# Optimization experiments

Hardware: AMD Instinct MI355X
Metric: run time of the kernel (lower is better)

## Reference

```python
import jax, jax.numpy as jnp
import numpy as np

B, C, T, H, W = 4, 256, 8, 32, 32
EPS = 1e-6


def setup_inputs() -> dict:
    key = jax.random.key(0)
    ks = jax.random.split(key, 8)
    s = 0.02  # init scale for 1x1 conv weights
    return {
        "x_motion": jax.random.normal(ks[0], (B, C, T, H, W), jnp.float32),
        "x_ref": jax.random.normal(ks[1], (B, C, 1, H, W), jnp.float32),
        "gamma": jnp.ones((C,), jnp.float32),
        "beta": jnp.zeros((C,), jnp.float32),
        "Wq": jax.random.normal(ks[2], (C, C), jnp.float32) * s,
        "bq": jnp.zeros((C,), jnp.float32),
        "Wk": jax.random.normal(ks[3], (C, C), jnp.float32) * s,
        "bk": jnp.zeros((C,), jnp.float32),
        "Wv": jax.random.normal(ks[4], (C, C), jnp.float32) * s,
        "bv": jnp.zeros((C,), jnp.float32),
        "Wo": jax.random.normal(ks[5], (C, C), jnp.float32) * s,
        "bo": jnp.zeros((C,), jnp.float32),
    }


def _group_norm(x, gamma, beta):
    # GroupNorm(num_groups=1): normalize over (C,T,H,W) per sample
    mu = jnp.mean(x, axis=(1, 2, 3, 4), keepdims=True)
    var = jnp.var(x, axis=(1, 2, 3, 4), keepdims=True)
    xn = (x - mu) * jax.lax.rsqrt(var + EPS)
    return xn * gamma[None, :, None, None, None] + beta[None, :, None, None, None]


def _conv1(x, Wmat, bias):
    # 1x1x1 Conv3d == per-position channel matmul
    return jnp.einsum('oc,bcthw->bothw', Wmat, x) + bias[None, :, None, None, None]


def reference(x_motion, x_ref, gamma, beta, Wq, bq, Wk, bk, Wv, bv, Wo, bo):
    h_mot = _group_norm(x_motion, gamma, beta)
    h_ref = _group_norm(x_ref, gamma, beta)
    q = _conv1(h_mot, Wq, bq)   # [b,c,t,h,w]
    k = _conv1(h_ref, Wk, bk)   # [b,c,1,h,w]
    v = _conv1(h_ref, Wv, bv)
    b, c, t, h, w = q.shape
    qf = q.transpose(0, 2, 3, 4, 1).reshape(b, t, h * w, c)   # [b,t,hw,c]
    kf = k[:, :, 0].transpose(0, 2, 3, 1).reshape(b, h * w, c)  # [b,hw,c]
    vf = v[:, :, 0].transpose(0, 2, 3, 1).reshape(b, h * w, c)
    # cross-attention: every frame attends to the single reference frame
    attn = jnp.einsum('btqc,bkc->btqk', qf, kf) * (c ** -0.5)
    attn = jax.nn.softmax(attn, axis=-1)
    out = jnp.einsum('btqk,bkc->btqc', attn, vf)
    out = out.reshape(b, t, h, w, c).transpose(0, 4, 1, 2, 3)  # [b,c,t,h,w]
    return x_motion + _conv1(out, Wo, bo)
```

## Files before the change

kernel.cpp:

```cpp
#include <hip/hip_runtime.h>
#include <math.h>
#include <stdint.h>

#define B_   4
#define C_   256
#define T_   8
#define HW_  1024
#define PM_  8192
#define PR_  1024
#define NM_  (C_ * PM_)
#define NR_  (C_ * PR_)
#define NBM  128
#define NBR  16
#define EPS_ 1e-6f

typedef unsigned short u16;
typedef unsigned int u32;
typedef __attribute__((ext_vector_type(8))) short short8;
typedef __attribute__((ext_vector_type(4))) float f32x4;

__device__ inline u16 f2bf(float f) {
    uint32_t u = __builtin_bit_cast(uint32_t, f);
    u += 0x7fffu + ((u >> 16) & 1u);
    return (u16)(u >> 16);
}
__device__ inline u32 pk2bf(float a, float b) {
    return (u32)f2bf(a) | ((u32)f2bf(b) << 16);
}

__device__ inline f32x4 mfma16(short8 a, short8 b, f32x4 c) {
    f32x4 d;
    asm("v_mfma_f32_16x16x32_bf16 %0, %1, %2, %3" : "=v"(d) : "v"(a), "v"(b), "0"(c));
    return d;
}
__device__ __forceinline__ short8 lds8(const char* p) {
    return __builtin_bit_cast(short8, *(const uint4*)p);
}
__device__ __forceinline__ void gl16(const void* g, void* l) {
    __builtin_amdgcn_global_load_lds(
        reinterpret_cast<const uint32_t __attribute__((address_space(1)))*>(
            reinterpret_cast<uintptr_t>(g)),
        reinterpret_cast<uint32_t __attribute__((address_space(3)))*>(
            reinterpret_cast<uintptr_t>(l)),
        16, 0, 0);
}

__global__ __launch_bounds__(256) void gn_stats(const float* __restrict__ x,
                                                int per_sample, int nblk,
                                                float* __restrict__ part) {
    int b   = blockIdx.x / nblk;
    int blk = blockIdx.x % nblk;
    const float* xb = x + (size_t)b * per_sample;
    int chunk = per_sample / nblk;
    int base  = blk * chunk;
    float s = 0.f, s2 = 0.f;
    for (int i = threadIdx.x * 4; i < chunk; i += 256 * 4) {
        float4 v = *(const float4*)(xb + base + i);
        s  += v.x + v.y + v.z + v.w;
        s2 += v.x * v.x + v.y * v.y + v.z * v.z + v.w * v.w;
    }
    #pragma unroll
    for (int off = 32; off; off >>= 1) {
        s  += __shfl_down(s, off);
        s2 += __shfl_down(s2, off);
    }
    __shared__ float red[8];
    int wid = threadIdx.x >> 6, lane = threadIdx.x & 63;
    if (lane == 0) { red[wid * 2] = s; red[wid * 2 + 1] = s2; }
    __syncthreads();
    if (threadIdx.x == 0) {
        for (int w = 1; w < 4; ++w) { s += red[w * 2]; s2 += red[w * 2 + 1]; }
        part[(size_t)(b * nblk + blk) * 2]     = s;
        part[(size_t)(b * nblk + blk) * 2 + 1] = s2;
    }
}

__global__ __launch_bounds__(256) void gn_finalize(const float* __restrict__ part_m,
                                                   const float* __restrict__ part_r,
                                                   const float* __restrict__ gamma,
                                                   const float* __restrict__ beta,
                                                   float* __restrict__ am, float* __restrict__ dm,
                                                   float* __restrict__ ar, float* __restrict__ dr) {
    int c = threadIdx.x;
    float g = gamma[c], be = beta[c];
    for (int b = 0; b < B_; ++b) {
        float s = 0.f, s2 = 0.f;
        for (int i = 0; i < NBM; ++i) { s += part_m[(b * NBM + i) * 2]; s2 += part_m[(b * NBM + i) * 2 + 1]; }
        float mu   = s / (float)NM_;
        float var  = s2 / (float)NM_ - mu * mu;
        float rstd = rsqrtf(var + EPS_);
        am[b * C_ + c] = rstd * g;
        dm[b * C_ + c] = be - mu * rstd * g;

        s = 0.f; s2 = 0.f;
        for (int i = 0; i < NBR; ++i) { s += part_r[(b * NBR + i) * 2]; s2 += part_r[(b * NBR + i) * 2 + 1]; }
        mu   = s / (float)NR_;
        var  = s2 / (float)NR_ - mu * mu;
        rstd = rsqrtf(var + EPS_);
        ar[b * C_ + c] = rstd * g;
        dr[b * C_ + c] = be - mu * rstd * g;
    }
}

__global__ __launch_bounds__(256) void w2bf(const float* __restrict__ W0,
                                            const float* __restrict__ W1,
                                            const float* __restrict__ W2,
                                            const float* __restrict__ W3,
                                            u16* __restrict__ dst) {
    int idx = blockIdx.x * 256 + threadIdx.x;
    int m = idx >> 13, off = (idx & 8191) * 8;
    const float* s = (m == 0 ? W0 : m == 1 ? W1 : m == 2 ? W2 : W3) + off;
    float4 a = *(const float4*)s, b = *(const float4*)(s + 4);
    ushort4 lo; lo.x = f2bf(a.x); lo.y = f2bf(a.y); lo.z = f2bf(a.z); lo.w = f2bf(a.w);
    ushort4 hi; hi.x = f2bf(b.x); hi.y = f2bf(b.y); hi.z = f2bf(b.z); hi.w = f2bf(b.w);
    *(ushort4*)(dst + m * 65536 + off)     = lo;
    *(ushort4*)(dst + m * 65536 + off + 4) = hi;
}

template<int P>
__global__ __launch_bounds__(256) void norm_tr(const float* __restrict__ X,
                                               const float* __restrict__ alpha,
                                               const float* __restrict__ delta,
                                               u16* __restrict__ Y) {
    __shared__ __align__(16) u16 S[64 * 256];
    int b = blockIdx.z, p0 = blockIdx.x * 64;
    int tid = threadIdx.x;
    #pragma unroll
    for (int pass = 0; pass < 4; ++pass) {
        int qi = pass * 256 + tid;
        int cq = qi & 63, pq = qi >> 6;
        float4 v[4];
        #pragma unroll
        for (int j = 0; j < 4; ++j) {
            int c = cq * 4 + j;
            v[j] = *(const float4*)(X + ((size_t)b * C_ + c) * P + p0 + pq * 4);
            float a = alpha[b * C_ + c], d = delta[b * C_ + c];
            v[j].x = v[j].x * a + d; v[j].y = v[j].y * a + d;
            v[j].z = v[j].z * a + d; v[j].w = v[j].w * a + d;
        }
        #pragma unroll
        for (int jj = 0; jj < 4; ++jj) {
            ushort4 o;
            o.x = f2bf(((const float*)&v[0])[jj]);
            o.y = f2bf(((const float*)&v[1])[jj]);
            o.z = f2bf(((const float*)&v[2])[jj]);
            o.w = f2bf(((const float*)&v[3])[jj]);
            *(ushort4*)&S[(pq * 4 + jj) * 256 + cq * 4] = o;
        }
    }
    __syncthreads();
    const char* Sb = (const char*)S;
    #pragma unroll
    for (int pass = 0; pass < 8; ++pass) {
        int i = pass * 256 + tid;
        int p = i >> 5, s = i & 31;
        uint4 d = *(const uint4*)(Sb + p * 512 + s * 16);
        *(uint4*)((char*)(Y + ((size_t)b * P + p0 + p) * C_) + s * 16) = d;
    }
}

template<int OUT>
__global__ __launch_bounds__(256) void convA(const u16* __restrict__ Xb,
                                             const u16* __restrict__ Wb,
                                             const float* __restrict__ bias,
                                             const float* __restrict__ resid,
                                             void* __restrict__ Yv,
                                             int P, float oscale) {
    __shared__ __align__(16) char lds[65536];
    int b = blockIdx.z, p0 = blockIdx.x * 64, o0 = blockIdx.y * 64;
    int tid = threadIdx.x, w = tid >> 6, l = tid & 63, lg = l >> 4, ln = l & 15;
    int wm = w >> 1, wn = w & 1;
    const char* Xg = (const char*)(Xb + ((size_t)b * P + p0) * C_);
    const char* Wg = (const char*)(Wb + (size_t)o0 * C_);
    #pragma unroll
    for (int i = 0; i < 8; ++i) {
        int ci = i * 4 + w;
        int d = ci * 1024 + l * 16;
        int srco = (d & ~511) | ((d & 511) ^ (((d >> 9) & 7) << 4));
        gl16(Xg + srco, lds + ci * 1024);
        gl16(Wg + srco, lds + 32768 + ci * 1024);
    }
    asm volatile("s_waitcnt vmcnt(0)" ::: "memory");
    __syncthreads();

    f32x4 acc[2][2];
    #pragma unroll
    for (int mm = 0; mm < 2; ++mm)
        #pragma unroll
        for (int nn = 0; nn < 2; ++nn) acc[mm][nn] = (f32x4)0.f;

    #pragma unroll
    for (int f = 0; f < 8; ++f) {
        short8 xf[2], wf[2];
        #pragma unroll
        for (int nn = 0; nn < 2; ++nn) {
            int p = wn * 32 + nn * 16 + ln;
            xf[nn] = lds8(lds + p * 512 + ((f * 64 + lg * 16) ^ ((p & 7) << 4)));
        }
        #pragma unroll
        for (int mm = 0; mm < 2; ++mm) {
            int o = wm * 32 + mm * 16 + ln;
            wf[mm] = lds8(lds + 32768 + o * 512 + ((f * 64 + lg * 16) ^ ((o & 7) << 4)));
        }
        #pragma unroll
        for (int mm = 0; mm < 2; ++mm)
            #pragma unroll
            for (int nn = 0; nn < 2; ++nn) {
                if (OUT == 1) acc[mm][nn] = mfma16(xf[nn], wf[mm], acc[mm][nn]);
                else          acc[mm][nn] = mfma16(wf[mm], xf[nn], acc[mm][nn]);
            }
    }
    __syncthreads();

    if constexpr (OUT == 0) {
        #pragma unroll
        for (int mm = 0; mm < 2; ++mm) {
            int obase = o0 + wm * 32 + mm * 16 + lg * 4;
            float b0 = bias[obase], b1 = bias[obase + 1], b2 = bias[obase + 2], b3 = bias[obase + 3];
            #pragma unroll
            for (int nn = 0; nn < 2; ++nn) {
                int pl = wn * 32 + nn * 16 + ln;
                int a = pl * 128 + ((wm * 64 + mm * 32 + lg * 8) ^ ((pl & 7) << 4));
                *(u32*)(lds + a)     = pk2bf((acc[mm][nn][0] + b0) * oscale, (acc[mm][nn][1] + b1) * oscale);
                *(u32*)(lds + a + 4) = pk2bf((acc[mm][nn][2] + b2) * oscale, (acc[mm][nn][3] + b3) * oscale);
            }
        }
        __syncthreads();
        u16* Y = (u16*)Yv;
        #pragma unroll
        for (int pass = 0; pass < 2; ++pass) {
            int i = pass * 256 + tid;
            int pl = i >> 3, s = i & 7;
            uint4 d = *(const uint4*)(lds + pl * 128 + ((s * 16) ^ ((pl & 7) << 4)));
            *(uint4*)(Y + (size_t)(b * P + p0 + pl) * C_ + o0 + s * 8) = d;
        }
    } else if constexpr (OUT == 1) {
        #pragma unroll
        for (int mm = 0; mm < 2; ++mm) {
            int ol = wm * 32 + mm * 16 + ln;
            float bo = bias[o0 + ol];
            #pragma unroll
            for (int nn = 0; nn < 2; ++nn) {
                int a = ol * 128 + ((wn * 64 + nn * 32 + lg * 8) ^ ((ol & 7) << 4));
                *(u32*)(lds + a)     = pk2bf(acc[mm][nn][0] + bo, acc[mm][nn][1] + bo);
                *(u32*)(lds + a + 4) = pk2bf(acc[mm][nn][2] + bo, acc[mm][nn][3] + bo);
            }
        }
        __syncthreads();
        u16* Y = (u16*)Yv;
        #pragma unroll
        for (int pass = 0; pass < 2; ++pass) {
            int i = pass * 256 + tid;
            int ol = i >> 3, s = i & 7;
            uint4 d = *(const uint4*)(lds + ol * 128 + ((s * 16) ^ ((ol & 7) << 4)));
            *(uint4*)(Y + (size_t)(b * C_ + o0 + ol) * P + p0 + s * 8) = d;
        }
    } else {
        #pragma unroll
        for (int mm = 0; mm < 2; ++mm) {
            int obase = wm * 32 + mm * 16 + lg * 4;
            #pragma unroll
            for (int r = 0; r < 4; ++r) {
                int ol = obase + r;
                float bo = bias[o0 + ol];
                #pragma unroll
                for (int nn = 0; nn < 2; ++nn) {
                    int a = ol * 256 + ((wn * 128 + nn * 64 + ln * 4) ^ ((ol & 7) << 4));
                    *(float*)(lds + a) = acc[mm][nn][r] + bo;
                }
            }
        }
        __syncthreads();
        float* Y = (float*)Yv;
        #pragma unroll
        for (int pass = 0; pass < 4; ++pass) {
            int i = pass * 256 + tid;
            int ol = i >> 4, s = i & 15;
            f32x4 dv = *(const f32x4*)(lds + ol * 256 + ((s * 16) ^ ((ol & 7) << 4)));
            size_t go = (size_t)(b * C_ + o0 + ol) * P + p0 + s * 4;
            float4 rv = *(const float4*)(resid + go);
            float4 o4;
            o4.x = dv[0] + rv.x; o4.y = dv[1] + rv.y; o4.z = dv[2] + rv.z; o4.w = dv[3] + rv.w;
            *(float4*)(Y + go) = o4;
        }
    }
}

__global__ __launch_bounds__(256) void attn2(const u16* __restrict__ qT,
                                             const u16* __restrict__ kT,
                                             const u16* __restrict__ vh,
                                             u16* __restrict__ ao) {
    __shared__ __align__(16) char lds[69632];
    int b = blockIdx.z, t = blockIdx.y, q0 = blockIdx.x * 64;
    int tid = threadIdx.x, w = tid >> 6, l = tid & 63, lg = l >> 4, ln = l & 15;

    const u16* Qrow = qT + ((size_t)b * PM_ + t * HW_ + q0 + w * 16 + ln) * C_;
    short8 qf[8];
    #pragma unroll
    for (int f = 0; f < 8; ++f)
        qf[f] = __builtin_bit_cast(short8, *(const uint4*)((const char*)Qrow + f * 64 + lg * 16));

    const char* Kb = (const char*)(kT + (size_t)b * PR_ * C_);
    const char* Vb = (const char*)(vh + (size_t)b * C_ * PR_);

    f32x4 acc[16];
    #pragma unroll
    for (int cc = 0; cc < 16; ++cc) acc[cc] = (f32x4)0.f;
    float m_r = -1e30f, l_r = 0.f;

    auto stage = [&](int buf, int kt) {
        const char* Kg = Kb + kt * 32 * 512;
        char* Kl = lds + buf * 16384;
        char* Vl = lds + 32768 + buf * 16384;
        #pragma unroll
        for (int i = 0; i < 4; ++i) {
            int ci = i * 4 + w;
            int d = ci * 1024 + l * 16;
            int srco = (d & ~511) | ((d & 511) ^ (((d >> 9) & 7) << 4));
            gl16(Kg + srco, Kl + ci * 1024);
        }
        #pragma unroll
        for (int i = 0; i < 4; ++i) {
            int ci = i * 4 + w;
            int d = ci * 1024 + l * 16;
            int c = d >> 6;
            int srco = c * 2048 + kt * 64 + ((d & 63) ^ (((c >> 1) & 3) << 4));
            gl16(Vb + srco, Vl + ci * 1024);
        }
    };

    stage(0, 0);
    asm volatile("s_waitcnt vmcnt(0)" ::: "memory");
    __syncthreads();

    char* Pl = lds + 65536 + w * 1024;
    for (int kt = 0; kt < 32; ++kt) {
        int buf = kt & 1;
        if (kt < 31) stage(buf ^ 1, kt + 1);
        const char* Kl = lds + buf * 16384;
        const char* Vl = lds + 32768 + buf * 16384;

        f32x4 s0 = (f32x4)0.f, s1 = (f32x4)0.f;
        #pragma unroll
        for (int f = 0; f < 8; ++f) {
            int r1 = 16 + ln;
            short8 k0f = lds8(Kl + ln * 512 + ((f * 64 + lg * 16) ^ ((ln & 7) << 4)));
            short8 k1f = lds8(Kl + r1 * 512 + ((f * 64 + lg * 16) ^ ((r1 & 7) << 4)));
            s0 = mfma16(k0f, qf[f], s0);
            s1 = mfma16(k1f, qf[f], s1);
        }

        float tm = fmaxf(fmaxf(fmaxf(s0[0], s0[1]), fmaxf(s0[2], s0[3])),
                         fmaxf(fmaxf(s1[0], s1[1]), fmaxf(s1[2], s1[3])));
        tm = fmaxf(tm, __shfl_xor(tm, 16));
        tm = fmaxf(tm, __shfl_xor(tm, 32));
        if (__any(tm > m_r + 8.f)) {
            float mn = fmaxf(m_r, tm);
            float sc = __expf(m_r - mn);
            m_r = mn; l_r *= sc;
            #pragma unroll
            for (int cc = 0; cc < 16; ++cc) {
                acc[cc][0] *= sc; acc[cc][1] *= sc; acc[cc][2] *= sc; acc[cc][3] *= sc;
            }
        }
        float p0v[4], p1v[4], rs = 0.f;
        #pragma unroll
        for (int r = 0; r < 4; ++r) { p0v[r] = __expf(s0[r] - m_r); rs += p0v[r]; }
        #pragma unroll
        for (int r = 0; r < 4; ++r) { p1v[r] = __expf(s1[r] - m_r); rs += p1v[r]; }
        rs += __shfl_xor(rs, 16);
        rs += __shfl_xor(rs, 32);
        l_r += rs;

        int sw = ((ln >> 1) & 3) << 4;
        int a0 = ln * 64 + ((lg * 8) ^ sw);
        *(u32*)(Pl + a0)     = pk2bf(p0v[0], p0v[1]);
        *(u32*)(Pl + a0 + 4) = pk2bf(p0v[2], p0v[3]);
        int a1 = ln * 64 + ((32 + lg * 8) ^ sw);
        *(u32*)(Pl + a1)     = pk2bf(p1v[0], p1v[1]);
        *(u32*)(Pl + a1 + 4) = pk2bf(p1v[2], p1v[3]);

        short8 pf = lds8(Pl + ln * 64 + ((lg * 16) ^ sw));

        #pragma unroll
        for (int cc = 0; cc < 16; ++cc) {
            int c = cc * 16 + ln;
            short8 vf = lds8(Vl + c * 64 + ((lg * 16) ^ (((c >> 1) & 3) << 4)));
            acc[cc] = mfma16(vf, pf, acc[cc]);
        }

        asm volatile("s_waitcnt vmcnt(0)" ::: "memory");
        __syncthreads();
    }

    float invl = 1.f / l_r;
    char* Os = lds;
    int qrow = w * 16 + ln;
    #pragma unroll
    for (int cc = 0; cc < 16; ++cc) {
        int a = qrow * 512 + ((cc * 32 + lg * 8) ^ ((qrow & 7) << 4));
        *(u32*)(Os + a)     = pk2bf(acc[cc][0] * invl, acc[cc][1] * invl);
        *(u32*)(Os + a + 4) = pk2bf(acc[cc][2] * invl, acc[cc][3] * invl);
    }
    __syncthreads();
    u16* aob = ao + ((size_t)b * PM_ + t * HW_ + q0) * C_;
    #pragma unroll
    for (int pass = 0; pass < 8; ++pass) {
        int i = pass * 256 + tid;
        int qr = i >> 5, s = i & 31;
        uint4 d = *(const uint4*)(Os + qr * 512 + ((s * 16) ^ ((qr & 7) << 4)));
        *(uint4*)((char*)(aob + (size_t)qr * C_) + s * 16) = d;
    }
}

extern "C" void kernel_launch(void* const* d_in, const int* in_sizes, int n_in,
                              void* d_out, int out_size, void* d_ws, size_t ws_size,
                              hipStream_t stream) {
    const float* x_motion = (const float*)d_in[0];
    const float* x_ref    = (const float*)d_in[1];
    const float* gamma    = (const float*)d_in[2];
    const float* beta     = (const float*)d_in[3];
    const float* Wq = (const float*)d_in[4];
    const float* bq = (const float*)d_in[5];
    const float* Wk = (const float*)d_in[6];
    const float* bk = (const float*)d_in[7];
    const float* Wv = (const float*)d_in[8];
    const float* bv = (const float*)d_in[9];
    const float* Wo = (const float*)d_in[10];
    const float* bo = (const float*)d_in[11];
    float* out = (float*)d_out;
    char* base = (char*)d_ws;

    float* part_m = (float*)(base);
    float* part_r = (float*)(base + 4096);
    float* am = (float*)(base + 8192);
    float* dm = (float*)(base + 12288);
    float* ar = (float*)(base + 16384);
    float* dr = (float*)(base + 20480);
    u16* wall = (u16*)(base + 32768);
    u16* wqb = wall;
    u16* wkb = wall + 65536;
    u16* wvb = wall + 131072;
    u16* wob = wall + 196608;
    u16* xnm = (u16*)(base + 1048576);
    u16* aoh = xnm;
    u16* xnr = (u16*)(base + 1048576 + 16777216);
    u16* qT  = (u16*)(base + 1048576 + 16777216 + 2097152);
    u16* kTp = (u16*)(base + 1048576 + 2 * 16777216 + 2097152);
    u16* vh  = (u16*)(base + 1048576 + 2 * 16777216 + 2 * 2097152);

    gn_stats<<<dim3(B_ * NBM), 256, 0, stream>>>(x_motion, NM_, NBM, part_m);
    gn_stats<<<dim3(B_ * NBR), 256, 0, stream>>>(x_ref, NR_, NBR, part_r);
    gn_finalize<<<dim3(1), 256, 0, stream>>>(part_m, part_r, gamma, beta, am, dm, ar, dr);
    w2bf<<<dim3(128), 256, 0, stream>>>(Wq, Wk, Wv, Wo, wall);

    norm_tr<PM_><<<dim3(PM_ / 64, 1, B_), 256, 0, stream>>>(x_motion, am, dm, xnm);
    norm_tr<PR_><<<dim3(PR_ / 64, 1, B_), 256, 0, stream>>>(x_ref, ar, dr, xnr);

    convA<0><<<dim3(PM_ / 64, 4, B_), 256, 0, stream>>>(xnm, wqb, bq, nullptr, qT, PM_, 0.0625f);
    convA<0><<<dim3(PR_ / 64, 4, B_), 256, 0, stream>>>(xnr, wkb, bk, nullptr, kTp, PR_, 1.f);
    convA<1><<<dim3(PR_ / 64, 4, B_), 256, 0, stream>>>(xnr, wvb, bv, nullptr, vh, PR_, 1.f);

    attn2<<<dim3(16, T_, B_), 256, 0, stream>>>(qT, kTp, vh, aoh);

    convA<2><<<dim3(PM_ / 64, 4, B_), 256, 0, stream>>>(aoh, wob, bo, x_motion, out, PM_, 1.f);
}
```

Baseline: 144.1 us.

## Merge small launches and rewrite attention with 32x32 MFMA and larger tiles

```diff
diff --git a/kernel.cpp b/kernel.cpp
--- a/kernel.cpp
+++ b/kernel.cpp
@@ -13,11 +13,13 @@
 #define NBM  128
 #define NBR  16
 #define EPS_ 1e-6f
+#define QSCALE 0.09016844f
 
 typedef unsigned short u16;
 typedef unsigned int u32;
 typedef __attribute__((ext_vector_type(8))) short short8;
 typedef __attribute__((ext_vector_type(4))) float f32x4;
+typedef __attribute__((ext_vector_type(16))) float f32x16;
 
 __device__ inline u16 f2bf(float f) {
     uint32_t u = __builtin_bit_cast(uint32_t, f);
@@ -31,6 +33,11 @@
 __device__ inline f32x4 mfma16(short8 a, short8 b, f32x4 c) {
     f32x4 d;
     asm("v_mfma_f32_16x16x32_bf16 %0, %1, %2, %3" : "=v"(d) : "v"(a), "v"(b), "0"(c));
+    return d;
+}
+__device__ inline f32x16 mfma32(short8 a, short8 b, f32x16 c) {
+    f32x16 d;
+    asm("v_mfma_f32_32x32x16_bf16 %0, %1, %2, %3" : "=v"(d) : "v"(a), "v"(b), "0"(c));
     return d;
 }
 __device__ __forceinline__ short8 lds8(const char* p) {
@@ -45,11 +52,10 @@
         16, 0, 0);
 }
 
-__global__ __launch_bounds__(256) void gn_stats(const float* __restrict__ x,
-                                                int per_sample, int nblk,
-                                                float* __restrict__ part) {
-    int b   = blockIdx.x / nblk;
-    int blk = blockIdx.x % nblk;
+__device__ void gn_body(const float* __restrict__ x, int per_sample, int nblk,
+                        float* __restrict__ part, int bid) {
+    int b   = bid / nblk;
+    int blk = bid % nblk;
     const float* xb = x + (size_t)b * per_sample;
     int chunk = per_sample / nblk;
     int base  = blk * chunk;
@@ -74,39 +80,47 @@
         part[(size_t)(b * nblk + blk) * 2 + 1] = s2;
     }
 }
-
-__global__ __launch_bounds__(256) void gn_finalize(const float* __restrict__ part_m,
-                                                   const float* __restrict__ part_r,
-                                                   const float* __restrict__ gamma,
-                                                   const float* __restrict__ beta,
-                                                   float* __restrict__ am, float* __restrict__ dm,
-                                                   float* __restrict__ ar, float* __restrict__ dr) {
-    int c = threadIdx.x;
-    float g = gamma[c], be = beta[c];
-    for (int b = 0; b < B_; ++b) {
-        float s = 0.f, s2 = 0.f;
-        for (int i = 0; i < NBM; ++i) { s += part_m[(b * NBM + i) * 2]; s2 += part_m[(b * NBM + i) * 2 + 1]; }
-        float mu   = s / (float)NM_;
-        float var  = s2 / (float)NM_ - mu * mu;
-        float rstd = rsqrtf(var + EPS_);
-        am[b * C_ + c] = rstd * g;
-        dm[b * C_ + c] = be - mu * rstd * g;
-
-        s = 0.f; s2 = 0.f;
-        for (int i = 0; i < NBR; ++i) { s += part_r[(b * NBR + i) * 2]; s2 += part_r[(b * NBR + i) * 2 + 1]; }
-        mu   = s / (float)NR_;
-        var  = s2 / (float)NR_ - mu * mu;
-        rstd = rsqrtf(var + EPS_);
-        ar[b * C_ + c] = rstd * g;
-        dr[b * C_ + c] = be - mu * rstd * g;
-    }
-}
-
-__global__ __launch_bounds__(256) void w2bf(const float* __restrict__ W0,
-                                            const float* __restrict__ W1,
-                                            const float* __restrict__ W2,
-                                            const float* __restrict__ W3,
-                                            u16* __restrict__ dst) {
+__global__ __launch_bounds__(256) void gn_all(const float* __restrict__ xm,
+                                              const float* __restrict__ xr,
+                                              float* __restrict__ part_m,
+                                              float* __restrict__ part_r) {
+    if (blockIdx.x < 512) gn_body(xm, NM_, NBM, part_m, blockIdx.x);
+    else                  gn_body(xr, NR_, NBR, part_r, blockIdx.x - 512);
+}
+
+__global__ __launch_bounds__(256) void fin_w2bf(const float* __restrict__ part_m,
+                                                const float* __restrict__ part_r,
+                                                const float* __restrict__ gamma,
+                                                const float* __restrict__ beta,
+                                                float* __restrict__ am, float* __restrict__ dm,
+                                                float* __restrict__ ar, float* __restrict__ dr,
+                                                const float* __restrict__ W0,
+                                                const float* __restrict__ W1,
+                                                const float* __restrict__ W2,
+                                                const float* __restrict__ W3,
+                                                u16* __restrict__ dst) {
+    if (blockIdx.x == 128) {
+        int c = threadIdx.x;
+        float g = gamma[c], be = beta[c];
+        for (int b = 0; b < B_; ++b) {
+            float s = 0.f, s2 = 0.f;
+            for (int i = 0; i < NBM; ++i) { s += part_m[(b * NBM + i) * 2]; s2 += part_m[(b * NBM + i) * 2 + 1]; }
+            float mu   = s / (float)NM_;
+            float var  = s2 / (float)NM_ - mu * mu;
+            float rstd = rsqrtf(var + EPS_);
+            am[b * C_ + c] = rstd * g;
+            dm[b * C_ + c] = be - mu * rstd * g;
+
+            s = 0.f; s2 = 0.f;
+            for (int i = 0; i < NBR; ++i) { s += part_r[(b * NBR + i) * 2]; s2 += part_r[(b * NBR + i) * 2 + 1]; }
+            mu   = s / (float)NR_;
+            var  = s2 / (float)NR_ - mu * mu;
+            rstd = rsqrtf(var + EPS_);
+            ar[b * C_ + c] = rstd * g;
+            dr[b * C_ + c] = be - mu * rstd * g;
+        }
+        return;
+    }
     int idx = blockIdx.x * 256 + threadIdx.x;
     int m = idx >> 13, off = (idx & 8191) * 8;
     const float* s = (m == 0 ? W0 : m == 1 ? W1 : m == 2 ? W2 : W3) + off;
@@ -117,13 +131,12 @@
     *(ushort4*)(dst + m * 65536 + off + 4) = hi;
 }
 
-template<int P>
-__global__ __launch_bounds__(256) void norm_tr(const float* __restrict__ X,
-                                               const float* __restrict__ alpha,
-                                               const float* __restrict__ delta,
-                                               u16* __restrict__ Y) {
-    __shared__ __align__(16) u16 S[64 * 256];
-    int b = blockIdx.z, p0 = blockIdx.x * 64;
+__device__ void norm_body(const float* __restrict__ X,
+                          const float* __restrict__ alpha,
+                          const float* __restrict__ delta,
+                          u16* __restrict__ Y, int P, int px, int b,
+                          u16* S) {
+    int p0 = px * 64;
     int tid = threadIdx.x;
     #pragma unroll
     for (int pass = 0; pass < 4; ++pass) {
@@ -158,17 +171,29 @@
         *(uint4*)((char*)(Y + ((size_t)b * P + p0 + p) * C_) + s * 16) = d;
     }
 }
+__global__ __launch_bounds__(256) void norm_all(const float* __restrict__ xm,
+                                                const float* __restrict__ xr,
+                                                const float* __restrict__ am,
+                                                const float* __restrict__ dm,
+                                                const float* __restrict__ ar,
+                                                const float* __restrict__ dr,
+                                                u16* __restrict__ xnm,
+                                                u16* __restrict__ xnr) {
+    __shared__ __align__(16) u16 S[64 * 256];
+    int bid = blockIdx.x;
+    if (bid < 512) norm_body(xm, am, dm, xnm, PM_, bid & 127, bid >> 7, S);
+    else { int i = bid - 512; norm_body(xr, ar, dr, xnr, PR_, i & 15, i >> 4, S); }
+}
 
 template<int OUT>
-__global__ __launch_bounds__(256) void convA(const u16* __restrict__ Xb,
-                                             const u16* __restrict__ Wb,
-                                             const float* __restrict__ bias,
-                                             const float* __restrict__ resid,
-                                             void* __restrict__ Yv,
-                                             int P, float oscale) {
-    __shared__ __align__(16) char lds[65536];
-    int b = blockIdx.z, p0 = blockIdx.x * 64, o0 = blockIdx.y * 64;
-    int tid = threadIdx.x, w = tid >> 6, l = tid & 63, lg = l >> 4, ln = l & 15;
+__device__ void convA_body(char* lds,
+                           const u16* __restrict__ Xb, const u16* __restrict__ Wb,
+                           const float* __restrict__ bias, const float* __restrict__ resid,
+                           void* __restrict__ Yv, int P, float oscale,
+                           int px, int oy, int b) {
+    int p0 = px * 64, o0 = oy * 64;
+    int tid = threadIdx.x;
+    int w = tid >> 6, l = tid & 63, lg = l >> 4, ln = l & 15;
     int wm = w >> 1, wn = w & 1;
     const char* Xg = (const char*)(Xb + ((size_t)b * P + p0) * C_);
     const char* Wg = (const char*)(Wb + (size_t)o0 * C_);
@@ -286,45 +311,80 @@
     }
 }
 
-__global__ __launch_bounds__(256) void attn2(const u16* __restrict__ qT,
-                                             const u16* __restrict__ kT,
-                                             const u16* __restrict__ vh,
-                                             u16* __restrict__ ao) {
-    __shared__ __align__(16) char lds[69632];
-    int b = blockIdx.z, t = blockIdx.y, q0 = blockIdx.x * 64;
-    int tid = threadIdx.x, w = tid >> 6, l = tid & 63, lg = l >> 4, ln = l & 15;
-
-    const u16* Qrow = qT + ((size_t)b * PM_ + t * HW_ + q0 + w * 16 + ln) * C_;
-    short8 qf[8];
-    #pragma unroll
-    for (int f = 0; f < 8; ++f)
-        qf[f] = __builtin_bit_cast(short8, *(const uint4*)((const char*)Qrow + f * 64 + lg * 16));
+__global__ __launch_bounds__(256) void convQKV(const u16* __restrict__ xnm,
+                                               const u16* __restrict__ xnr,
+                                               const u16* __restrict__ wall,
+                                               const float* __restrict__ bq,
+                                               const float* __restrict__ bk,
+                                               const float* __restrict__ bv,
+                                               u16* __restrict__ qT,
+                                               u16* __restrict__ kT,
+                                               u16* __restrict__ vh) {
+    __shared__ __align__(16) char lds[65536];
+    int bid = blockIdx.x;
+    if (bid < 2048) {
+        convA_body<0>(lds, xnm, wall, bq, nullptr, qT, PM_, QSCALE,
+                      bid & 127, (bid >> 7) & 3, bid >> 9);
+    } else if (bid < 2304) {
+        int i = bid - 2048;
+        convA_body<0>(lds, xnr, wall + 65536, bk, nullptr, kT, PR_, 1.f,
+                      i & 15, (i >> 4) & 3, i >> 6);
+    } else {
+        int i = bid - 2304;
+        convA_body<1>(lds, xnr, wall + 131072, bv, nullptr, vh, PR_, 1.f,
+                      i & 15, (i >> 4) & 3, i >> 6);
+    }
+}
+
+__global__ __launch_bounds__(256) void convO(const u16* __restrict__ aoh,
+                                             const u16* __restrict__ wall,
+                                             const float* __restrict__ bo,
+                                             const float* __restrict__ resid,
+                                             float* __restrict__ out) {
+    __shared__ __align__(16) char lds[65536];
+    convA_body<2>(lds, aoh, wall + 196608, bo, resid, out, PM_, 1.f,
+                  blockIdx.x, blockIdx.y, blockIdx.z);
+}
+
+__global__ __launch_bounds__(256, 1) void attn4(const u16* __restrict__ qT,
+                                                const u16* __restrict__ kT,
+                                                const u16* __restrict__ vh,
+                                                u16* __restrict__ ao) {
+    __shared__ __align__(16) char lds[147456];
+    int b = blockIdx.z, t = blockIdx.y, q0 = blockIdx.x * 128;
+    int tid = threadIdx.x, w = tid >> 6, l = tid & 63;
+    int m31 = l & 31, hi = l >> 5;
+
+    const char* Qrow = (const char*)(qT + ((size_t)b * PM_ + t * HW_ + q0 + w * 32 + m31) * C_);
+    short8 qf[16];
+    #pragma unroll
+    for (int ch = 0; ch < 16; ++ch)
+        qf[ch] = __builtin_bit_cast(short8, *(const uint4*)(Qrow + ch * 32 + hi * 16));
 
     const char* Kb = (const char*)(kT + (size_t)b * PR_ * C_);
     const char* Vb = (const char*)(vh + (size_t)b * C_ * PR_);
 
-    f32x4 acc[16];
-    #pragma unroll
-    for (int cc = 0; cc < 16; ++cc) acc[cc] = (f32x4)0.f;
+    f32x16 acc[8];
+    #pragma unroll
+    for (int cb = 0; cb < 8; ++cb) acc[cb] = (f32x16)0.f;
     float m_r = -1e30f, l_r = 0.f;
 
     auto stage = [&](int buf, int kt) {
-        const char* Kg = Kb + kt * 32 * 512;
-        char* Kl = lds + buf * 16384;
-        char* Vl = lds + 32768 + buf * 16384;
-        #pragma unroll
-        for (int i = 0; i < 4; ++i) {
+        char* Kl = lds + buf * 32768;
+        char* Vl = lds + 65536 + buf * 32768;
+        #pragma unroll
+        for (int i = 0; i < 8; ++i) {
             int ci = i * 4 + w;
             int d = ci * 1024 + l * 16;
             int srco = (d & ~511) | ((d & 511) ^ (((d >> 9) & 7) << 4));
-            gl16(Kg + srco, Kl + ci * 1024);
-        }
-        #pragma unroll
-        for (int i = 0; i < 4; ++i) {
+            gl16(Kb + (size_t)kt * 32768 + srco, Kl + ci * 1024);
+        }
+        #pragma unroll
+        for (int i = 0; i < 8; ++i) {
             int ci = i * 4 + w;
             int d = ci * 1024 + l * 16;
-            int c = d >> 6;
-            int srco = c * 2048 + kt * 64 + ((d & 63) ^ (((c >> 1) & 3) << 4));
+            int c = d >> 7, s = (d >> 4) & 7;
+            int srco = c * 2048 + kt * 128 + ((s * 16) ^ ((c & 7) << 4));
             gl16(Vb + srco, Vl + ci * 1024);
         }
     };
@@ -333,79 +393,94 @@
     asm volatile("s_waitcnt vmcnt(0)" ::: "memory");
     __syncthreads();
 
-    char* Pl = lds + 65536 + w * 1024;
-    for (int kt = 0; kt < 32; ++kt) {
+    char* Pw = lds + 131072 + w * 4096;
+    int swzp = (m31 & 7) << 4;
+
+    for (int kt = 0; kt < 16; ++kt) {
         int buf = kt & 1;
-        if (kt < 31) stage(buf ^ 1, kt + 1);
-        const char* Kl = lds + buf * 16384;
-        const char* Vl = lds + 32768 + buf * 16384;
-
-        f32x4 s0 = (f32x4)0.f, s1 = (f32x4)0.f;
-        #pragma unroll
-        for (int f = 0; f < 8; ++f) {
-            int r1 = 16 + ln;
-            short8 k0f = lds8(Kl + ln * 512 + ((f * 64 + lg * 16) ^ ((ln & 7) << 4)));
-            short8 k1f = lds8(Kl + r1 * 512 + ((f * 64 + lg * 16) ^ ((r1 & 7) << 4)));
-            s0 = mfma16(k0f, qf[f], s0);
-            s1 = mfma16(k1f, qf[f], s1);
-        }
-
-        float tm = fmaxf(fmaxf(fmaxf(s0[0], s0[1]), fmaxf(s0[2], s0[3])),
-                         fmaxf(fmaxf(s1[0], s1[1]), fmaxf(s1[2], s1[3])));
-        tm = fmaxf(tm, __shfl_xor(tm, 16));
-        tm = fmaxf(tm, __shfl_xor(tm, 32));
+        if (kt < 15) stage(buf ^ 1, kt + 1);
+        const char* Kl = lds + buf * 32768;
+        const char* Vl = lds + 65536 + buf * 32768;
+
+        f32x16 s0 = (f32x16)0.f, s1 = (f32x16)0.f;
+        #pragma unroll
+        for (int ch = 0; ch < 16; ++ch) {
+            int off = (ch * 32 + hi * 16) ^ swzp;
+            short8 k0f = lds8(Kl + m31 * 512 + off);
+            short8 k1f = lds8(Kl + (32 + m31) * 512 + off);
+            s0 = mfma32(k0f, qf[ch], s0);
+            s1 = mfma32(k1f, qf[ch], s1);
+        }
+
+        float tm = -1e30f;
+        #pragma unroll
+        for (int e = 0; e < 16; ++e) tm = fmaxf(tm, fmaxf(s0[e], s1[e]));
         if (__any(tm > m_r + 8.f)) {
-            float mn = fmaxf(m_r, tm);
-            float sc = __expf(m_r - mn);
-            m_r = mn; l_r *= sc;
+            float tmax = fmaxf(tm, __shfl_xor(tm, 32));
+            float mn = fmaxf(m_r, tmax);
+            float sc = __builtin_amdgcn_exp2f(m_r - mn);
+            l_r *= sc;
             #pragma unroll
-            for (int cc = 0; cc < 16; ++cc) {
-                acc[cc][0] *= sc; acc[cc][1] *= sc; acc[cc][2] *= sc; acc[cc][3] *= sc;
+            for (int cb = 0; cb < 8; ++cb)
+                #pragma unroll
+                for (int e = 0; e < 16; ++e) acc[cb][e] *= sc;
+            m_r = mn;
+        }
+        float p0[16], p1[16], rs = 0.f;
+        #pragma unroll
+        for (int e = 0; e < 16; ++e) { p0[e] = __builtin_amdgcn_exp2f(s0[e] - m_r); rs += p0[e]; }
+        #pragma unroll
+        for (int e = 0; e < 16; ++e) { p1[e] = __builtin_amdgcn_exp2f(s1[e] - m_r); rs += p1[e]; }
+        l_r += rs;
+
+        #pragma unroll
+        for (int a = 0; a < 8; ++a) {
+            const float* parr = (a < 4) ? p0 : p1;
+            int eb = (a & 3) * 4;
+            uint2 d;
+            d.x = pk2bf(parr[eb + 0], parr[eb + 1]);
+            d.y = pk2bf(parr[eb + 2], parr[eb + 3]);
+            *(uint2*)(Pw + m31 * 128 + ((a * 16 + hi * 8) ^ swzp)) = d;
+        }
+
+        short8 bP[4];
+        #pragma unroll
+        for (int kc = 0; kc < 4; ++kc)
+            bP[kc] = lds8(Pw + m31 * 128 + ((kc * 32 + hi * 16) ^ swzp));
+
+        #pragma unroll
+        for (int cb = 0; cb < 8; ++cb) {
+            int c = cb * 32 + m31;
+            int rowb = c * 128, swzc = (c & 7) << 4;
+            #pragma unroll
+            for (int kc = 0; kc < 4; ++kc) {
+                short8 vf = lds8(Vl + rowb + ((kc * 32 + hi * 16) ^ swzc));
+                acc[cb] = mfma32(vf, bP[kc], acc[cb]);
             }
-        }
-        float p0v[4], p1v[4], rs = 0.f;
-        #pragma unroll
-        for (int r = 0; r < 4; ++r) { p0v[r] = __expf(s0[r] - m_r); rs += p0v[r]; }
-        #pragma unroll
-        for (int r = 0; r < 4; ++r) { p1v[r] = __expf(s1[r] - m_r); rs += p1v[r]; }
-        rs += __shfl_xor(rs, 16);
-        rs += __shfl_xor(rs, 32);
-        l_r += rs;
-
-        int sw = ((ln >> 1) & 3) << 4;
-        int a0 = ln * 64 + ((lg * 8) ^ sw);
-        *(u32*)(Pl + a0)     = pk2bf(p0v[0], p0v[1]);
-        *(u32*)(Pl + a0 + 4) = pk2bf(p0v[2], p0v[3]);
-        int a1 = ln * 64 + ((32 + lg * 8) ^ sw);
-        *(u32*)(Pl + a1)     = pk2bf(p1v[0], p1v[1]);
-        *(u32*)(Pl + a1 + 4) = pk2bf(p1v[2], p1v[3]);
-
-        short8 pf = lds8(Pl + ln * 64 + ((lg * 16) ^ sw));
-
-        #pragma unroll
-        for (int cc = 0; cc < 16; ++cc) {
-            int c = cc * 16 + ln;
-            short8 vf = lds8(Vl + c * 64 + ((lg * 16) ^ (((c >> 1) & 3) << 4)));
-            acc[cc] = mfma16(vf, pf, acc[cc]);
         }
 
         asm volatile("s_waitcnt vmcnt(0)" ::: "memory");
         __syncthreads();
     }
 
+    l_r += __shfl_xor(l_r, 32);
     float invl = 1.f / l_r;
     char* Os = lds;
-    int qrow = w * 16 + ln;
-    #pragma unroll
-    for (int cc = 0; cc < 16; ++cc) {
-        int a = qrow * 512 + ((cc * 32 + lg * 8) ^ ((qrow & 7) << 4));
-        *(u32*)(Os + a)     = pk2bf(acc[cc][0] * invl, acc[cc][1] * invl);
-        *(u32*)(Os + a + 4) = pk2bf(acc[cc][2] * invl, acc[cc][3] * invl);
-    }
+    int q = w * 32 + m31;
+    int swzq = (q & 7) << 4;
+    #pragma unroll
+    for (int cb = 0; cb < 8; ++cb)
+        #pragma unroll
+        for (int m = 0; m < 4; ++m) {
+            uint2 d;
+            d.x = pk2bf(acc[cb][4 * m + 0] * invl, acc[cb][4 * m + 1] * invl);
+            d.y = pk2bf(acc[cb][4 * m + 2] * invl, acc[cb][4 * m + 3] * invl);
+            *(uint2*)(Os + q * 512 + ((cb * 64 + m * 16 + hi * 8) ^ swzq)) = d;
+        }
     __syncthreads();
     u16* aob = ao + ((size_t)b * PM_ + t * HW_ + q0) * C_;
     #pragma unroll
-    for (int pass = 0; pass < 8; ++pass) {
+    for (int pass = 0; pass < 16; ++pass) {
         int i = pass * 256 + tid;
         int qr = i >> 5, s = i & 31;
         uint4 d = *(const uint4*)(Os + qr * 512 + ((s * 16) ^ ((qr & 7) << 4)));
@@ -438,10 +513,6 @@
     float* ar = (float*)(base + 16384);
     float* dr = (float*)(base + 20480);
     u16* wall = (u16*)(base + 32768);
-    u16* wqb = wall;
-    u16* wkb = wall + 65536;
-    u16* wvb = wall + 131072;
-    u16* wob = wall + 196608;
     u16* xnm = (u16*)(base + 1048576);
     u16* aoh = xnm;
     u16* xnr = (u16*)(base + 1048576 + 16777216);
@@ -449,19 +520,11 @@
     u16* kTp = (u16*)(base + 1048576 + 2 * 16777216 + 2097152);
     u16* vh  = (u16*)(base + 1048576 + 2 * 16777216 + 2 * 2097152);
 
-    gn_stats<<<dim3(B_ * NBM), 256, 0, stream>>>(x_motion, NM_, NBM, part_m);
-    gn_stats<<<dim3(B_ * NBR), 256, 0, stream>>>(x_ref, NR_, NBR, part_r);
-    gn_finalize<<<dim3(1), 256, 0, stream>>>(part_m, part_r, gamma, beta, am, dm, ar, dr);
-    w2bf<<<dim3(128), 256, 0, stream>>>(Wq, Wk, Wv, Wo, wall);
-
-    norm_tr<PM_><<<dim3(PM_ / 64, 1, B_), 256, 0, stream>>>(x_motion, am, dm, xnm);
-    norm_tr<PR_><<<dim3(PR_ / 64, 1, B_), 256, 0, stream>>>(x_ref, ar, dr, xnr);
-
-    convA<0><<<dim3(PM_ / 64, 4, B_), 256, 0, stream>>>(xnm, wqb, bq, nullptr, qT, PM_, 0.0625f);
-    convA<0><<<dim3(PR_ / 64, 4, B_), 256, 0, stream>>>(xnr, wkb, bk, nullptr, kTp, PR_, 1.f);
-    convA<1><<<dim3(PR_ / 64, 4, B_), 256, 0, stream>>>(xnr, wvb, bv, nullptr, vh, PR_, 1.f);
-
-    attn2<<<dim3(16, T_, B_), 256, 0, stream>>>(qT, kTp, vh, aoh);
-
-    convA<2><<<dim3(PM_ / 64, 4, B_), 256, 0, stream>>>(aoh, wob, bo, x_motion, out, PM_, 1.f);
-}
+    gn_all<<<dim3(576), 256, 0, stream>>>(x_motion, x_ref, part_m, part_r);
+    fin_w2bf<<<dim3(129), 256, 0, stream>>>(part_m, part_r, gamma, beta,
+                                            am, dm, ar, dr, Wq, Wk, Wv, Wo, wall);
+    norm_all<<<dim3(576), 256, 0, stream>>>(x_motion, x_ref, am, dm, ar, dr, xnm, xnr);
+    convQKV<<<dim3(2560), 256, 0, stream>>>(xnm, xnr, wall, bq, bk, bv, qT, kTp, vh);
+    attn4<<<dim3(8, T_, B_), 256, 0, stream>>>(qT, kTp, vh, aoh);
+    convO<<<dim3(PM_ / 64, 4, B_), 256, 0, stream>>>(aoh, wall, bo, x_motion, out);
+}
```

Result: faster. 127.9 us (-11.3%).
